# Kernel tuning notes

Hardware: AMD Instinct MI355X
Metric: run time of the kernel (lower is better)

Reference implementation:

```python
import jax, jax.numpy as jnp
import numpy as np

N_STREAMS = 4
TAU = 1.0
ALPHA = 0.1
CAYLEY_ITERS = 2
LN_EPS = 1e-5


def setup_inputs() -> dict:
    key = jax.random.key(0)
    k1, k2, k3 = jax.random.split(key, 3)
    b, l, d = 2, 4096, 2048
    n = N_STREAMS
    x = jax.random.normal(k1, (b, l, d), dtype=jnp.float32)
    ln_w = jnp.ones((d,), dtype=jnp.float32)
    ln_b = jnp.zeros((d,), dtype=jnp.float32)
    # CastedLinear: trunc_normal std = 1/sqrt(in_features)
    proj_w = jax.random.truncated_normal(k2, -2.0, 2.0, (3 * n * n, d), dtype=jnp.float32) / jnp.sqrt(d * 1.0)
    proj_b = jnp.zeros((3 * n * n,), dtype=jnp.float32)
    # sublayer_fn realized as a dense linear (typical transformer sublayer core)
    W_sub = jax.random.normal(k3, (d, d), dtype=jnp.float32) / jnp.sqrt(d * 1.0)
    return {"x": x, "ln_w": ln_w, "ln_b": ln_b, "proj_w": proj_w, "proj_b": proj_b, "W_sub": W_sub}


def _layernorm(x, w, b):
    mu = jnp.mean(x, axis=-1, keepdims=True)
    var = jnp.mean(jnp.square(x - mu), axis=-1, keepdims=True)
    return (x - mu) * jax.lax.rsqrt(var + LN_EPS) * w + b


def _iterative_cayley(raw):
    # raw: (b, l, n, n) fp32
    w = raw - jnp.swapaxes(raw, -1, -2)
    eye = jnp.eye(N_STREAMS, dtype=raw.dtype)
    y = eye + ALPHA * w
    for _ in range(CAYLEY_ITERS):
        y = eye + 0.5 * ALPHA * jnp.matmul(w, eye + y)
    return y


def reference(x, ln_w, ln_b, proj_w, proj_b, W_sub):
    b, l, d = x.shape
    n = N_STREAMS
    gates = _layernorm(x, ln_w, ln_b) @ proj_w.T + proj_b  # (b, l, 3*n*n)
    pre_raw, post_raw, res_raw = jnp.split(gates, 3, axis=-1)
    pre_raw = pre_raw.reshape(b, l, n, n).astype(jnp.float32)
    post_raw = post_raw.reshape(b, l, n, n).astype(jnp.float32)
    res_raw = res_raw.reshape(b, l, n, n).astype(jnp.float32)
    h_pre = jax.nn.softmax(pre_raw / TAU, axis=-1)
    h_post = jax.nn.softmax(post_raw / TAU, axis=-2)
    h_res = _iterative_cayley(res_raw)
    # All streams of x_streams are identical copies of x, so
    # einsum('blij,bljd->blid', h, x_streams).mean(-2) == mean_i(sum_j h[i,j]) * x.
    coeff_pre = jnp.mean(jnp.sum(h_pre, axis=-1), axis=-1)    # (b, l)
    coeff_res = jnp.mean(jnp.sum(h_res, axis=-1), axis=-1)    # (b, l)
    coeff_post = jnp.mean(jnp.sum(h_post, axis=-1), axis=-1)  # (b, l)
    x_in = coeff_pre[..., None] * x
    y = x_in @ W_sub  # sublayer_fn
    return coeff_res[..., None] * x + coeff_post[..., None] * y
```

## Files before the change

kernel.cpp:

```cpp
#include <hip/hip_runtime.h>
#include <stdint.h>


typedef __attribute__((ext_vector_type(8))) __bf16 bf16x8;
typedef __attribute__((ext_vector_type(4))) float f32x4;
typedef __attribute__((ext_vector_type(8))) unsigned short us8;
typedef __attribute__((ext_vector_type(4))) unsigned short us4;

__device__ __forceinline__ unsigned short f2bf(float f) {
  union { float f; unsigned int u; } v; v.f = f;
  unsigned int u = v.u;
  u += 0x7fffu + ((u >> 16) & 1u);
  return (unsigned short)(u >> 16);
}

__device__ __forceinline__ void gload_lds16(const void* g, void* l) {
  __builtin_amdgcn_global_load_lds(
      (__attribute__((address_space(1))) void*)g,
      (__attribute__((address_space(3))) void*)l, 16, 0, 0);
}

__global__ __launch_bounds__(256) void k_ln_conv(
    const float* __restrict__ x, const float* __restrict__ lw, const float* __restrict__ lb,
    unsigned short* __restrict__ xb, unsigned short* __restrict__ lnb, int D) {
  const int t = blockIdx.x;
  const int tid = threadIdx.x;
  const float* row = x + (size_t)t * D;
  f32x4 a = *(const f32x4*)(row + tid * 8);
  f32x4 b = *(const f32x4*)(row + tid * 8 + 4);
  float vv[8] = {a[0], a[1], a[2], a[3], b[0], b[1], b[2], b[3]};
  float s = 0.f, ss = 0.f;
#pragma unroll
  for (int j = 0; j < 8; ++j) { s += vv[j]; ss += vv[j] * vv[j]; }
#pragma unroll
  for (int off = 32; off > 0; off >>= 1) { s += __shfl_down(s, off); ss += __shfl_down(ss, off); }
  __shared__ float red[8];
  __shared__ float st[2];
  int lane = tid & 63, wv = tid >> 6;
  if (lane == 0) { red[wv] = s; red[4 + wv] = ss; }
  __syncthreads();
  if (tid == 0) {
    float S = red[0] + red[1] + red[2] + red[3];
    float SS = red[4] + red[5] + red[6] + red[7];
    float mu = S / (float)D;
    float var = SS / (float)D - mu * mu;
    st[0] = mu; st[1] = rsqrtf(var + 1e-5f);
  }
  __syncthreads();
  float mu = st[0], rstd = st[1];
  f32x4 w0 = *(const f32x4*)(lw + tid * 8), w1 = *(const f32x4*)(lw + tid * 8 + 4);
  f32x4 b0 = *(const f32x4*)(lb + tid * 8), b1 = *(const f32x4*)(lb + tid * 8 + 4);
  float ww[8] = {w0[0], w0[1], w0[2], w0[3], w1[0], w1[1], w1[2], w1[3]};
  float bb[8] = {b0[0], b0[1], b0[2], b0[3], b1[0], b1[1], b1[2], b1[3]};
  us8 ox, ol;
#pragma unroll
  for (int j = 0; j < 8; ++j) {
    ox[j] = f2bf(vv[j]);
    ol[j] = f2bf((vv[j] - mu) * rstd * ww[j] + bb[j]);
  }
  *(us8*)(xb + (size_t)t * D + tid * 8) = ox;
  *(us8*)(lnb + (size_t)t * D + tid * 8) = ol;
}

__global__ __launch_bounds__(256) void k_wt(const float* __restrict__ W,
                                            unsigned short* __restrict__ Wt, int D) {
  __shared__ float tile[64][65];
  int kb = blockIdx.x * 64, nb = blockIdx.y * 64;
  int tid = threadIdx.x;
  int tx = tid & 15, ty = tid >> 4;
#pragma unroll
  for (int p = 0; p < 4; ++p) {
    int r = p * 16 + ty;
    f32x4 v = *(const f32x4*)(W + (size_t)(kb + r) * D + nb + tx * 4);
    tile[r][tx * 4 + 0] = v[0]; tile[r][tx * 4 + 1] = v[1];
    tile[r][tx * 4 + 2] = v[2]; tile[r][tx * 4 + 3] = v[3];
  }
  __syncthreads();
#pragma unroll
  for (int p = 0; p < 2; ++p) {
    int c = p * 256 + tid;
    int nr = c >> 3, kc = (c & 7) * 8;
    us8 o;
#pragma unroll
    for (int j = 0; j < 8; ++j) o[j] = f2bf(tile[kc + j][nr]);
    *(us8*)(Wt + (size_t)(nb + nr) * D + kb + kc) = o;
  }
}

__global__ void k_pconv(const float* __restrict__ p, unsigned short* __restrict__ q, int n) {
  int i = (blockIdx.x * 256 + threadIdx.x) * 4;
  if (i < n) {
    f32x4 v = *(const f32x4*)(p + i);
    us4 o;
#pragma unroll
    for (int j = 0; j < 4; ++j) o[j] = f2bf(v[j]);
    *(us4*)(q + i) = o;
  }
}

__global__ __launch_bounds__(256) void k_gates(
    const unsigned short* __restrict__ A,
    const unsigned short* __restrict__ Bp,
    const float* __restrict__ pb,
    float* __restrict__ cresp, float* __restrict__ cpyp, int K) {
  __shared__ __attribute__((aligned(16))) unsigned short As[128 * 32];
  __shared__ __attribute__((aligned(16))) unsigned short Bs[48 * 32];
  __shared__ float gl[128][49];
  __shared__ float pbs[48];
  int tid = threadIdx.x, lane = tid & 63, wv = tid >> 6;
  if (tid < 48) pbs[tid] = pb[tid];
  f32x4 acc[2][3] = {};
  size_t rowBase = (size_t)blockIdx.x * 128;
  for (int k0 = 0; k0 < K; k0 += 32) {
#pragma unroll
    for (int inst = 0; inst < 2; ++inst) {
      int eo = inst * 2048 + wv * 512 + lane * 8;
      int r = eo >> 5, cc = eo & 31;
      gload_lds16(A + (rowBase + r) * K + k0 + cc, (char*)As + inst * 4096 + wv * 1024);
    }
    if (tid < 192) {
      int r = tid >> 2, cc = (tid & 3) * 8;
      us8 v = *(const us8*)(Bp + (size_t)r * K + k0 + cc);
      *(us8*)(Bs + r * 32 + cc) = v;
    }
    __syncthreads();
    int kb = (lane >> 4) * 8, rr = lane & 15;
    bf16x8 av[2], bv[3];
#pragma unroll
    for (int mi = 0; mi < 2; ++mi)
      av[mi] = *(const bf16x8*)(As + (wv * 32 + mi * 16 + rr) * 32 + kb);
#pragma unroll
    for (int ni = 0; ni < 3; ++ni)
      bv[ni] = *(const bf16x8*)(Bs + (ni * 16 + rr) * 32 + kb);
#pragma unroll
    for (int mi = 0; mi < 2; ++mi)
#pragma unroll
      for (int ni = 0; ni < 3; ++ni)
        acc[mi][ni] = __builtin_amdgcn_mfma_f32_16x16x32_bf16(av[mi], bv[ni], acc[mi][ni], 0, 0, 0);
    __syncthreads();
  }
#pragma unroll
  for (int mi = 0; mi < 2; ++mi)
#pragma unroll
    for (int ni = 0; ni < 3; ++ni)
#pragma unroll
      for (int i = 0; i < 4; ++i)
        gl[wv * 32 + mi * 16 + (lane >> 4) * 4 + i][ni * 16 + (lane & 15)] = acc[mi][ni][i];
  __syncthreads();
  if (tid < 128) {
    float g[48];
#pragma unroll
    for (int j = 0; j < 48; ++j) g[j] = gl[tid][j] + pbs[j];
    float cpre = 0.f;
#pragma unroll
    for (int i = 0; i < 4; ++i) {
      float m = fmaxf(fmaxf(g[i * 4], g[i * 4 + 1]), fmaxf(g[i * 4 + 2], g[i * 4 + 3]));
      float e0 = expf(g[i * 4] - m), e1 = expf(g[i * 4 + 1] - m);
      float e2 = expf(g[i * 4 + 2] - m), e3 = expf(g[i * 4 + 3] - m);
      float inv = 1.f / (e0 + e1 + e2 + e3);
      cpre += e0 * inv + e1 * inv + e2 * inv + e3 * inv;
    }
    cpre *= 0.25f;
    float cpost = 0.f;
#pragma unroll
    for (int j = 0; j < 4; ++j) {
      float a0 = g[16 + j], a1 = g[20 + j], a2 = g[24 + j], a3 = g[28 + j];
      float m = fmaxf(fmaxf(a0, a1), fmaxf(a2, a3));
      float e0 = expf(a0 - m), e1 = expf(a1 - m), e2 = expf(a2 - m), e3 = expf(a3 - m);
      float inv = 1.f / (e0 + e1 + e2 + e3);
      cpost += e0 * inv + e1 * inv + e2 * inv + e3 * inv;
    }
    cpost *= 0.25f;
    float w4[16], y4[16];
#pragma unroll
    for (int i = 0; i < 4; ++i)
#pragma unroll
      for (int j = 0; j < 4; ++j)
        w4[i * 4 + j] = g[32 + i * 4 + j] - g[32 + j * 4 + i];
#pragma unroll
    for (int i = 0; i < 16; ++i) y4[i] = 0.1f * w4[i];
    y4[0] += 1.f; y4[5] += 1.f; y4[10] += 1.f; y4[15] += 1.f;
#pragma unroll
    for (int it = 0; it < 2; ++it) {
      float z[16];
#pragma unroll
      for (int i = 0; i < 16; ++i) z[i] = y4[i];
      z[0] += 1.f; z[5] += 1.f; z[10] += 1.f; z[15] += 1.f;
#pragma unroll
      for (int i = 0; i < 4; ++i)
#pragma unroll
        for (int j = 0; j < 4; ++j) {
          float acc2 = 0.f;
#pragma unroll
          for (int k = 0; k < 4; ++k) acc2 += w4[i * 4 + k] * z[k * 4 + j];
          y4[i * 4 + j] = ((i == j) ? 1.f : 0.f) + 0.05f * acc2;
        }
    }
    float cr = 0.f;
#pragma unroll
    for (int i = 0; i < 16; ++i) cr += y4[i];
    cr *= 0.25f;
    cresp[rowBase + tid] = cr;
    cpyp[rowBase + tid] = cpre * cpost;
  }
}

__global__ __launch_bounds__(512, 2) void k_gemm(
    const unsigned short* __restrict__ A,
    const unsigned short* __restrict__ Bt,
    const float* __restrict__ x,
    const float* __restrict__ cresp, const float* __restrict__ cpyp,
    float* __restrict__ out, int M, int N, int K) {
  __shared__ __attribute__((aligned(16))) unsigned short As[4][256 * 32];
  __shared__ __attribute__((aligned(16))) unsigned short Bs[4][256 * 32];
  const int tid = threadIdx.x, lane = tid & 63, wv = tid >> 6;
  const int nbn = N >> 8;
  const int nwg = (M >> 8) * nbn;
  const int chunk = nwg >> 3;
  const int gid = (blockIdx.x & 7) * chunk + (blockIdx.x >> 3);
  const int bm = gid / nbn, bn = gid % nbn;
  const int wm = wv >> 2, wn = wv & 3;
  const int rr = lane & 15, ksl = lane >> 4;
  const int koff = (ksl ^ ((rr >> 1) & 3)) * 8;
  const int rloc = tid >> 2;
  const int cbelem = ((tid & 3) ^ ((tid >> 3) & 3)) * 8;
  const unsigned short* aG = A + (size_t)((bm << 8) + rloc) * K + cbelem;
  const unsigned short* bG = Bt + (size_t)((bn << 8) + rloc) * K + cbelem;
  f32x4 acc[8][4] = {};
  const int nsl = K >> 5;

#define STAGE(KT, SLOT)                                                        \
  {                                                                            \
    const unsigned short* ag_ = aG + (KT) * 32;                                \
    const unsigned short* bg_ = bG + (KT) * 32;                                \
    unsigned short* la_ = &As[(SLOT)][wv * 512];                               \
    unsigned short* lb_ = &Bs[(SLOT)][wv * 512];                               \
    gload_lds16(ag_, la_);                                                     \
    gload_lds16(ag_ + (size_t)128 * K, la_ + 4096);                            \
    gload_lds16(bg_, lb_);                                                     \
    gload_lds16(bg_ + (size_t)128 * K, lb_ + 4096);                            \
  }

#define REGION(S, BVC, BVN)                                                    \
  {                                                                            \
    asm volatile("s_waitcnt vmcnt(4)" ::: "memory");                           \
    __builtin_amdgcn_sched_barrier(0);                                         \
    __builtin_amdgcn_s_barrier();                                              \
    __builtin_amdgcn_sched_barrier(0);                                         \
    int kt_ = jb + (S) + 3;                                                    \
    if (kt_ > nsl - 1) kt_ = nsl - 1;                                          \
    STAGE(kt_, ((S) + 3) & 3)                                                  \
    __builtin_amdgcn_sched_barrier(0);                                         \
    const unsigned short* Ab = &As[(S) & 3][(wm * 128 + rr) * 32 + koff];      \
    bf16x8 av[8];                                                              \
    _Pragma("unroll")                                                          \
    for (int mf = 0; mf < 8; ++mf) av[mf] = *(const bf16x8*)(Ab + mf * 512);   \
    const unsigned short* Bb = &Bs[((S) + 1) & 3][(wn * 64 + rr) * 32 + koff]; \
    _Pragma("unroll")                                                          \
    for (int nf = 0; nf < 4; ++nf) BVN[nf] = *(const bf16x8*)(Bb + nf * 512);  \
    __builtin_amdgcn_s_setprio(1);                                             \
    _Pragma("unroll")                                                          \
    for (int mf = 0; mf < 8; ++mf)                                             \
      _Pragma("unroll")                                                        \
      for (int nf = 0; nf < 4; ++nf)                                           \
        acc[mf][nf] = __builtin_amdgcn_mfma_f32_16x16x32_bf16(                 \
            av[mf], BVC[nf], acc[mf][nf], 0, 0, 0);                            \
    __builtin_amdgcn_s_setprio(0);                                             \
  }

  bf16x8 bvP[4], bvQ[4];
  STAGE(0, 0)
  STAGE(1, 1)
  STAGE(2, 2)
  asm volatile("s_waitcnt vmcnt(8)" ::: "memory");
  __builtin_amdgcn_sched_barrier(0);
  __builtin_amdgcn_s_barrier();
  {
    const unsigned short* Bb = &Bs[0][(wn * 64 + rr) * 32 + koff];
#pragma unroll
    for (int nf = 0; nf < 4; ++nf) bvP[nf] = *(const bf16x8*)(Bb + nf * 512);
  }
  for (int jb = 0; jb < nsl; jb += 4) {
    REGION(0, bvP, bvQ)
    REGION(1, bvQ, bvP)
    REGION(2, bvP, bvQ)
    REGION(3, bvQ, bvP)
  }
#undef REGION
#undef STAGE

  const int orow0 = (bm << 8) + wm * 128 + ksl * 4;
  const int ocol0 = (bn << 8) + wn * 64 + rr;
#pragma unroll
  for (int mf = 0; mf < 8; ++mf)
#pragma unroll
    for (int i = 0; i < 4; ++i) {
      const int row = orow0 + mf * 16 + i;
      const float crv = cresp[row], cpv = cpyp[row];
      const size_t base = (size_t)row * N + ocol0;
#pragma unroll
      for (int nf = 0; nf < 4; ++nf)
        out[base + nf * 16] = crv * x[base + nf * 16] + cpv * acc[mf][nf][i];
    }
}

extern "C" void kernel_launch(void* const* d_in, const int* in_sizes, int n_in,
                              void* d_out, int out_size, void* d_ws, size_t ws_size,
                              hipStream_t stream) {
  const float* x  = (const float*)d_in[0];
  const float* lw = (const float*)d_in[1];
  const float* lb = (const float*)d_in[2];
  const float* pw = (const float*)d_in[3];
  const float* pb = (const float*)d_in[4];
  const float* W  = (const float*)d_in[5];
  float* out = (float*)d_out;

  const int D = in_sizes[1];
  const int M = in_sizes[0] / D;
  const int G = in_sizes[4];

  char* ws = (char*)d_ws;
  size_t off = 0;
  unsigned short* xb  = (unsigned short*)(ws + off); off += (size_t)M * D * 2;
  unsigned short* lnb = (unsigned short*)(ws + off); off += (size_t)M * D * 2;
  unsigned short* Wt  = (unsigned short*)(ws + off); off += (size_t)D * D * 2;
  unsigned short* pjb = (unsigned short*)(ws + off); off += (size_t)G * D * 2;
  float* cres = (float*)(ws + off); off += (size_t)M * 4;
  float* cpy  = (float*)(ws + off); off += (size_t)M * 4;

  k_ln_conv<<<M, 256, 0, stream>>>(x, lw, lb, xb, lnb, D);
  k_wt<<<dim3(D / 64, D / 64), 256, 0, stream>>>(W, Wt, D);
  k_pconv<<<(G * D / 4 + 255) / 256, 256, 0, stream>>>(pw, pjb, G * D);
  k_gates<<<M / 128, 256, 0, stream>>>(lnb, pjb, pb, cres, cpy, D);

  const int nwg = (M / 256) * (D / 256);
  k_gemm<<<nwg, 512, 0, stream>>>(xb, Wt, x, cres, cpy, out, M, D, D);
}
```

Measured before the change: 143.5 us.

## Double-buffer A fragments in GEMM registers and read bf16 residual in epilogue

Each pipeline region of the GEMM main loop now prefetches both the A and B fragments for the next k-slice into registers and then issues MFMAs on the current ones, so LDS read latency for A is hidden behind compute. Before, only B was double-buffered. The epilogue now reads the residual x from the bf16 copy already in the workspace instead of the fp32 input, which halves that read traffic. In exchange, register pressure rises from two sets of A fragments, which may force spills under launch_bounds(512,2). The residual term also loses precision because it is rounded to bf16.

After: 137.0 us. -4.5%, faster.

```diff
diff --git a/kernel.cpp b/kernel.cpp
--- a/kernel.cpp
+++ b/kernel.cpp
@@ -12,6 +12,11 @@
   unsigned int u = v.u;
   u += 0x7fffu + ((u >> 16) & 1u);
   return (unsigned short)(u >> 16);
+}
+
+__device__ __forceinline__ float bf2f(unsigned short u) {
+  union { unsigned int u; float f; } v; v.u = (unsigned int)u << 16;
+  return v.f;
 }
 
 __device__ __forceinline__ void gload_lds16(const void* g, void* l) {
@@ -208,7 +213,7 @@
 __global__ __launch_bounds__(512, 2) void k_gemm(
     const unsigned short* __restrict__ A,
     const unsigned short* __restrict__ Bt,
-    const float* __restrict__ x,
+    const unsigned short* __restrict__ xbr,
     const float* __restrict__ cresp, const float* __restrict__ cpyp,
     float* __restrict__ out, int M, int N, int K) {
   __shared__ __attribute__((aligned(16))) unsigned short As[4][256 * 32];
@@ -241,7 +246,9 @@
     gload_lds16(bg_ + (size_t)128 * K, lb_ + 4096);                            \
   }
 
-#define REGION(S, BVC, BVN)                                                    \
+  bf16x8 avA[8], bvA[4], avB[8], bvB[4];
+
+#define REGION(S, CAV, CBV, NAV, NBV)                                          \
   {                                                                            \
     asm volatile("s_waitcnt vmcnt(4)" ::: "memory");                           \
     __builtin_amdgcn_sched_barrier(0);                                         \
@@ -251,24 +258,23 @@
     if (kt_ > nsl - 1) kt_ = nsl - 1;                                          \
     STAGE(kt_, ((S) + 3) & 3)                                                  \
     __builtin_amdgcn_sched_barrier(0);                                         \
-    const unsigned short* Ab = &As[(S) & 3][(wm * 128 + rr) * 32 + koff];      \
-    bf16x8 av[8];                                                              \
+    const unsigned short* Abn = &As[((S) + 1) & 3][(wm * 128 + rr) * 32 + koff]; \
+    const unsigned short* Bbn = &Bs[((S) + 1) & 3][(wn * 64 + rr) * 32 + koff];  \
     _Pragma("unroll")                                                          \
-    for (int mf = 0; mf < 8; ++mf) av[mf] = *(const bf16x8*)(Ab + mf * 512);   \
-    const unsigned short* Bb = &Bs[((S) + 1) & 3][(wn * 64 + rr) * 32 + koff]; \
+    for (int mf = 0; mf < 8; ++mf) NAV[mf] = *(const bf16x8*)(Abn + mf * 512); \
     _Pragma("unroll")                                                          \
-    for (int nf = 0; nf < 4; ++nf) BVN[nf] = *(const bf16x8*)(Bb + nf * 512);  \
+    for (int nf = 0; nf < 4; ++nf) NBV[nf] = *(const bf16x8*)(Bbn + nf * 512); \
+    __builtin_amdgcn_sched_barrier(0);                                         \
     __builtin_amdgcn_s_setprio(1);                                             \
     _Pragma("unroll")                                                          \
     for (int mf = 0; mf < 8; ++mf)                                             \
       _Pragma("unroll")                                                        \
       for (int nf = 0; nf < 4; ++nf)                                           \
         acc[mf][nf] = __builtin_amdgcn_mfma_f32_16x16x32_bf16(                 \
-            av[mf], BVC[nf], acc[mf][nf], 0, 0, 0);                            \
+            CAV[mf], CBV[nf], acc[mf][nf], 0, 0, 0);                           \
     __builtin_amdgcn_s_setprio(0);                                             \
   }
 
-  bf16x8 bvP[4], bvQ[4];
   STAGE(0, 0)
   STAGE(1, 1)
   STAGE(2, 2)
@@ -276,15 +282,18 @@
   __builtin_amdgcn_sched_barrier(0);
   __builtin_amdgcn_s_barrier();
   {
-    const unsigned short* Bb = &Bs[0][(wn * 64 + rr) * 32 + koff];
-#pragma unroll
-    for (int nf = 0; nf < 4; ++nf) bvP[nf] = *(const bf16x8*)(Bb + nf * 512);
+    const unsigned short* Ab0 = &As[0][(wm * 128 + rr) * 32 + koff];
+    const unsigned short* Bb0 = &Bs[0][(wn * 64 + rr) * 32 + koff];
+#pragma unroll
+    for (int mf = 0; mf < 8; ++mf) avA[mf] = *(const bf16x8*)(Ab0 + mf * 512);
+#pragma unroll
+    for (int nf = 0; nf < 4; ++nf) bvA[nf] = *(const bf16x8*)(Bb0 + nf * 512);
   }
   for (int jb = 0; jb < nsl; jb += 4) {
-    REGION(0, bvP, bvQ)
-    REGION(1, bvQ, bvP)
-    REGION(2, bvP, bvQ)
-    REGION(3, bvQ, bvP)
+    REGION(0, avA, bvA, avB, bvB)
+    REGION(1, avB, bvB, avA, bvA)
+    REGION(2, avA, bvA, avB, bvB)
+    REGION(3, avB, bvB, avA, bvA)
   }
 #undef REGION
 #undef STAGE
@@ -300,7 +309,7 @@
       const size_t base = (size_t)row * N + ocol0;
 #pragma unroll
       for (int nf = 0; nf < 4; ++nf)
-        out[base + nf * 16] = crv * x[base + nf * 16] + cpv * acc[mf][nf][i];
+        out[base + nf * 16] = crv * bf2f(xbr[base + nf * 16]) + cpv * acc[mf][nf][i];
     }
 }
 
@@ -334,5 +343,5 @@
   k_gates<<<M / 128, 256, 0, stream>>>(lnb, pjb, pb, cres, cpy, D);
 
   const int nwg = (M / 256) * (D / 256);
-  k_gemm<<<nwg, 512, 0, stream>>>(xb, Wt, x, cres, cpy, out, M, D, D);
-}
+  k_gemm<<<nwg, 512, 0, stream>>>(xb, Wt, xb, cres, cpy, out, M, D, D);
+}
```
